# Kernel tuning notes

Measured on AMD Instinct MI355X. Metric: run time of the kernel, lower is better.

Reference implementation:

```python
import jax, jax.numpy as jnp
import numpy as np

B, T, V, D, C, O = 64, 128, 32, 128, 10000, 512


def setup_inputs() -> dict:
    key = jax.random.key(0)
    ks = jax.random.split(key, 14)
    s = 1.0 / np.sqrt(D)
    # ragged visit sequences: codes in [1, C), padded visits are all-zero codes
    codes = jax.random.randint(ks[0], (B, T, V), 1, C, dtype=jnp.int32)
    lengths = jax.random.randint(ks[1], (B,), 1, T + 1, dtype=jnp.int32)
    visit_mask = (jnp.arange(T)[None, :] < lengths[:, None])
    codes_x = codes * visit_mask[:, :, None].astype(jnp.int32)
    emb = (jax.random.normal(ks[2], (C, D), jnp.float32) * 0.02).at[0].set(0.0)
    return {
        "codes_x": codes_x,
        "emb": emb,
        "a_kernel": jax.random.normal(ks[3], (D, 3 * D), jnp.float32) * s,
        "a_rec": jax.random.normal(ks[4], (D, 3 * D), jnp.float32) * s,
        "a_bias": jnp.zeros((2, 3 * D), jnp.float32),
        "b_kernel": jax.random.normal(ks[5], (D, 3 * D), jnp.float32) * s,
        "b_rec": jax.random.normal(ks[6], (D, 3 * D), jnp.float32) * s,
        "b_bias": jnp.zeros((2, 3 * D), jnp.float32),
        "alpha_w": jax.random.normal(ks[7], (D, 1), jnp.float32) * s,
        "alpha_b": jnp.zeros((1,), jnp.float32),
        "beta_w": jax.random.normal(ks[8], (D, D), jnp.float32) * s,
        "beta_b": jnp.zeros((D,), jnp.float32),
        "cls_w": jax.random.normal(ks[9], (D, O), jnp.float32) * s,
        "cls_b": jnp.zeros((O,), jnp.float32),
    }


def gru(x, mask, kernel, rec, bias):
    """Keras GRU (reset_after=True), masked: carries state+output through padded steps.
    x: [B,T,D], mask: [B,T] bool -> [B,T,D]."""
    bi, br = bias[0], bias[1]
    xp = x @ kernel + bi  # [B,T,3D] precomputed input projection

    def step(h, inp):
        xp_t, m_t = inp
        hp = h @ rec + br
        xz, xr, xh = jnp.split(xp_t, 3, axis=-1)
        hz, hr, hh = jnp.split(hp, 3, axis=-1)
        z = jax.nn.sigmoid(xz + hz)
        r = jax.nn.sigmoid(xr + hr)
        hcand = jnp.tanh(xh + r * hh)
        h_new = z * h + (1.0 - z) * hcand
        h_out = jnp.where(m_t[:, None], h_new, h)
        return h_out, h_out

    h0 = jnp.zeros((x.shape[0], rec.shape[0]), x.dtype)
    _, ys = jax.lax.scan(step, h0, (jnp.swapaxes(xp, 0, 1), jnp.swapaxes(mask, 0, 1)))
    return jnp.swapaxes(ys, 0, 1)


def retain_forward(codes_x, emb, a_kernel, a_rec, a_bias, b_kernel, b_rec, b_bias,
                   alpha_w, alpha_b, beta_w, beta_b, cls_w, cls_b):
    x = emb[codes_x].sum(axis=2)                     # [B,T,D] visit embeddings
    mask = x.sum(axis=-1) != 0                       # [B,T] visit mask
    lengths = mask.sum(axis=-1)                      # [B]
    # masked reverse: rx[b, j] = x[b, lengths[b]-1-j] for j < lengths[b], else 0
    t = x.shape[1]
    idx = lengths[:, None] - 1 - jnp.arange(t)[None, :]  # [B,T]
    valid = idx >= 0
    rx = jnp.take_along_axis(x, jnp.clip(idx, 0, t - 1)[:, :, None], axis=1)
    rx = rx * valid[:, :, None].astype(x.dtype)
    # dual GRU attention (dropout inactive at inference)
    g = gru(rx, mask, a_kernel, a_rec, a_bias)
    h = gru(rx, mask, b_kernel, b_rec, b_bias)
    attn_alpha = jax.nn.softmax(g @ alpha_w + alpha_b, axis=1)   # [B,T,1]
    attn_beta = jnp.tanh(h @ beta_w + beta_b)                    # [B,T,D]
    c = jnp.sum(attn_alpha * attn_beta * x, axis=1)              # [B,D]
    return c @ cls_w + cls_b                                     # [B,O]


def reference(codes_x, emb, a_kernel, a_rec, a_bias, b_kernel, b_rec, b_bias,
              alpha_w, alpha_b, beta_w, beta_b, cls_w, cls_b):
    return retain_forward(codes_x, emb, a_kernel, a_rec, a_bias, b_kernel, b_rec,
                          b_bias, alpha_w, alpha_b, beta_w, beta_b, cls_w, cls_b)
```

## Files before the change

kernel.cpp:

```cpp
#include <hip/hip_runtime.h>
#include <math.h>

#define BATCH 64
#define TT 128
#define VV 32
#define DD 128
#define OO 512
#define N3 384
#define NN 768

#define OFF_X      0u
#define OFF_XPC    1048576u
#define OFF_GSEQ   7340032u
#define OFF_HSEQ   8388608u
#define OFF_INTS   9437184u
#define OFF_ALPHA  9453632u
#define OFF_CPART  9461824u

__global__ __launch_bounds__(128) void k_gather(const int* __restrict__ codes,
        const float* __restrict__ emb, float* __restrict__ x, int* __restrict__ mask) {
    int bt = blockIdx.x;
    int d = threadIdx.x;
    const int* cp = codes + (size_t)bt * VV;
    float acc = 0.f;
    #pragma unroll 8
    for (int v = 0; v < VV; ++v) {
        int code = cp[v];
        acc += emb[(size_t)code * DD + d];
    }
    x[(size_t)bt * DD + d] = acc;
    float s = acc;
    #pragma unroll
    for (int off = 32; off; off >>= 1) s += __shfl_xor(s, off);
    __shared__ float red[2];
    if ((d & 63) == 0) red[d >> 6] = s;
    __syncthreads();
    if (d == 0) mask[bt] = ((red[0] + red[1]) != 0.0f) ? 1 : 0;
}

__global__ __launch_bounds__(128) void k_len(const int* __restrict__ mask,
        int* __restrict__ lengths, int* __restrict__ ridx) {
    int b = blockIdx.x, t = threadIdx.x;
    int m = mask[b * TT + t];
    unsigned long long bal = __ballot(m != 0);
    __shared__ int cnt[2];
    if ((t & 63) == 0) cnt[t >> 6] = __popcll(bal);
    __syncthreads();
    int len = cnt[0] + cnt[1];
    if (t == 0) lengths[b] = len;
    ridx[b * TT + t] = len - 1 - t;
}

__global__ __launch_bounds__(256) void k_xp(const float* __restrict__ x,
        const float* __restrict__ akern, const float* __restrict__ bkern,
        const float* __restrict__ abias, const float* __restrict__ bbias,
        float* __restrict__ xpc) {
    __shared__ __attribute__((aligned(16))) float As[32][68];
    __shared__ __attribute__((aligned(16))) float Bs[32][68];
    int mb = blockIdx.x, nb = blockIdx.y;
    int n0 = nb * 64;
    int tid = threadIdx.x;
    int tx = tid & 15, ty = tid >> 4;
    float acc[4][4] = {};
    for (int k0 = 0; k0 < DD; k0 += 32) {
        #pragma unroll
        for (int i = 0; i < 2; ++i) {
            int s = tid * 2 + i;
            int row = s >> 3, kk = (s & 7) * 4;
            float4 v = *reinterpret_cast<const float4*>(x + (size_t)(mb * 64 + row) * DD + k0 + kk);
            As[kk][row] = v.x; As[kk+1][row] = v.y; As[kk+2][row] = v.z; As[kk+3][row] = v.w;
        }
        #pragma unroll
        for (int i = 0; i < 2; ++i) {
            int s = tid * 2 + i;
            int kk = s >> 4, c = (s & 15) * 4;
            int n = n0 + c;
            const float* src = (n < N3) ? (akern + (size_t)(k0 + kk) * N3 + n)
                                        : (bkern + (size_t)(k0 + kk) * N3 + (n - N3));
            *reinterpret_cast<float4*>(&Bs[kk][c]) = *reinterpret_cast<const float4*>(src);
        }
        __syncthreads();
        #pragma unroll
        for (int kk = 0; kk < 32; ++kk) {
            float4 a = *reinterpret_cast<const float4*>(&As[kk][ty * 4]);
            float4 bv = *reinterpret_cast<const float4*>(&Bs[kk][tx * 4]);
            float av[4] = {a.x, a.y, a.z, a.w};
            float bw[4] = {bv.x, bv.y, bv.z, bv.w};
            #pragma unroll
            for (int i2 = 0; i2 < 4; ++i2)
                #pragma unroll
                for (int j2 = 0; j2 < 4; ++j2)
                    acc[i2][j2] = fmaf(av[i2], bw[j2], acc[i2][j2]);
        }
        __syncthreads();
    }
    int nbase = n0 + tx * 4;
    float4 bias;
    if (nbase < N3) bias = *reinterpret_cast<const float4*>(abias + nbase);
    else            bias = *reinterpret_cast<const float4*>(bbias + (nbase - N3));
    #pragma unroll
    for (int i2 = 0; i2 < 4; ++i2) {
        int m = mb * 64 + ty * 4 + i2;
        float4 o;
        o.x = acc[i2][0] + bias.x; o.y = acc[i2][1] + bias.y;
        o.z = acc[i2][2] + bias.z; o.w = acc[i2][3] + bias.w;
        *reinterpret_cast<float4*>(xpc + (size_t)m * NN + nbase) = o;
    }
}

__device__ __forceinline__ float fast_sigmoid(float x) {
    return 1.f / (1.f + __expf(-x));
}
__device__ __forceinline__ float fast_tanh(float x) {
    float xc = fminf(fmaxf(x, -15.f), 15.f);
    float e2 = __expf(2.f * xc);
    return (e2 - 1.f) / (e2 + 1.f);
}

#define LOADW(i) float4 w##i; { const float* rp = rec + (size_t)(k0 + 4 * i) * N3 + j; \
    w##i.x = rp[0]; w##i.y = rp[N3]; w##i.z = rp[2 * N3]; w##i.w = rp[3 * N3]; }
#define DOTW(i) { float4 hv = *reinterpret_cast<const float4*>(&h_lds[k0 + 4 * i]); \
    a0 = fmaf(hv.x, w##i.x, a0); a1 = fmaf(hv.y, w##i.y, a1); \
    a2 = fmaf(hv.z, w##i.z, a2); a3 = fmaf(hv.w, w##i.w, a3); }

__global__ __launch_bounds__(768) __attribute__((amdgpu_waves_per_eu(3, 3)))
void k_gru(
        const float* __restrict__ arec, const float* __restrict__ abias,
        const float* __restrict__ brec, const float* __restrict__ bbias,
        const float* __restrict__ xpc, const int* __restrict__ mask,
        const int* __restrict__ ridx, float* __restrict__ gseq, float* __restrict__ hseq) {
    int b = blockIdx.x & 63;
    int gru = blockIdx.x >> 6;
    const float* rec  = gru ? brec : arec;
    const float* bias = gru ? bbias : abias;
    float* seq = gru ? hseq : gseq;
    int t = threadIdx.x;
    int half = (t >= N3) ? 1 : 0;
    int j = t - half * N3;
    int k0 = half * 64;
    LOADW(0)  LOADW(1)  LOADW(2)  LOADW(3)
    LOADW(4)  LOADW(5)  LOADW(6)  LOADW(7)
    LOADW(8)  LOADW(9)  LOADW(10) LOADW(11)
    LOADW(12) LOADW(13) LOADW(14) LOADW(15)
    __shared__ __attribute__((aligned(16))) float h_lds[DD];
    __shared__ float part[768];
    __shared__ int smask[TT];
    __shared__ int sridx[TT];
    if (t < TT) { smask[t] = mask[b * TT + t]; sridx[t] = ridx[b * TT + t]; }
    if (t < DD) h_lds[t] = 0.f;
    float bz_r = 0.f, br_r = 0.f, bh_r = 0.f, bz_i = 0.f, br_i = 0.f, bh_i = 0.f;
    if (t < DD) {
        bz_r = bias[N3 + t];  br_r = bias[N3 + DD + t];  bh_r = bias[N3 + 2 * DD + t];
        bz_i = bias[t];       br_i = bias[DD + t];       bh_i = bias[2 * DD + t];
    }
    float hreg = 0.f;
    __syncthreads();
    const float* xpb = xpc + (size_t)b * TT * NN + gru * N3;
    for (int step = 0; step < TT; ++step) {
        int m = smask[step];
        if (!m) {
            if (t < DD) seq[(size_t)(b * TT + step) * DD + t] = hreg;
            continue;
        }
        float xz = 0.f, xr = 0.f, xh = 0.f;
        if (t < DD) {
            int row = sridx[step];
            if (row >= 0) {
                const float* xrow = xpb + (size_t)row * NN;
                xz = xrow[t]; xr = xrow[DD + t]; xh = xrow[2 * DD + t];
            } else {
                xz = bz_i; xr = br_i; xh = bh_i;
            }
        }
        float a0 = 0.f, a1 = 0.f, a2 = 0.f, a3 = 0.f;
        DOTW(0)  DOTW(1)  DOTW(2)  DOTW(3)
        DOTW(4)  DOTW(5)  DOTW(6)  DOTW(7)
        DOTW(8)  DOTW(9)  DOTW(10) DOTW(11)
        DOTW(12) DOTW(13) DOTW(14) DOTW(15)
        part[t] = (a0 + a1) + (a2 + a3);
        __syncthreads();
        if (t < DD) {
            float hz = part[t]           + part[t + N3]          + bz_r;
            float hr = part[t + DD]      + part[t + N3 + DD]     + br_r;
            float hh = part[t + 2 * DD]  + part[t + N3 + 2 * DD] + bh_r;
            float z = fast_sigmoid(xz + hz);
            float r = fast_sigmoid(xr + hr);
            float hc = fast_tanh(xh + r * hh);
            float hnew = z * hreg + (1.f - z) * hc;
            hreg = hnew;
            h_lds[t] = hnew;
            seq[(size_t)(b * TT + step) * DD + t] = hnew;
        }
        __syncthreads();
    }
}

__global__ __launch_bounds__(128) void k_alpha(const float* __restrict__ gseq,
        const float* __restrict__ alpha_w, const float* __restrict__ alpha_b,
        float* __restrict__ alpha) {
    int b = blockIdx.x, t = threadIdx.x;
    __shared__ float aw[DD];
    aw[t] = alpha_w[t];
    __syncthreads();
    const float* g = gseq + (size_t)(b * TT + t) * DD;
    float acc = 0.f;
    #pragma unroll
    for (int k = 0; k < DD; k += 4) {
        float4 gv = *reinterpret_cast<const float4*>(g + k);
        acc = fmaf(gv.x, aw[k],     acc);
        acc = fmaf(gv.y, aw[k + 1], acc);
        acc = fmaf(gv.z, aw[k + 2], acc);
        acc = fmaf(gv.w, aw[k + 3], acc);
    }
    float logit = acc + alpha_b[0];
    float mx = logit;
    #pragma unroll
    for (int off = 32; off; off >>= 1) mx = fmaxf(mx, __shfl_xor(mx, off));
    __shared__ float redm[2];
    if ((t & 63) == 0) redm[t >> 6] = mx;
    __syncthreads();
    mx = fmaxf(redm[0], redm[1]);
    float e = expf(logit - mx);
    float s = e;
    #pragma unroll
    for (int off = 32; off; off >>= 1) s += __shfl_xor(s, off);
    __shared__ float reds[2];
    if ((t & 63) == 0) reds[t >> 6] = s;
    __syncthreads();
    alpha[b * TT + t] = e / (reds[0] + reds[1]);
}

__global__ __launch_bounds__(128) void k_beta(const float* __restrict__ hseq,
        const float* __restrict__ x, const float* __restrict__ beta_w,
        const float* __restrict__ beta_b, const float* __restrict__ alpha,
        float* __restrict__ cpart) {
    __shared__ __attribute__((aligned(16))) float bw[DD][DD];
    __shared__ __attribute__((aligned(16))) float hr[4][DD];
    __shared__ float cred[4][DD];
    int b = blockIdx.x >> 3, grp = blockIdx.x & 7;
    int tid = threadIdx.x;
    for (int i = tid; i < DD * DD / 4; i += 128) {
        float4 v = *reinterpret_cast<const float4*>(beta_w + (size_t)i * 4);
        *reinterpret_cast<float4*>(&bw[0][0] + (size_t)i * 4) = v;
    }
    int trow = tid >> 5, dq = (tid & 31) * 4;
    float bb0 = beta_b[dq], bb1 = beta_b[dq + 1], bb2 = beta_b[dq + 2], bb3 = beta_b[dq + 3];
    float c0 = 0.f, c1 = 0.f, c2 = 0.f, c3 = 0.f;
    for (int tg = 0; tg < 4; ++tg) {
        int t = grp * 16 + tg * 4 + trow;
        size_t rowoff = (size_t)(b * TT + t) * DD;
        float4 hv = *reinterpret_cast<const float4*>(hseq + rowoff + dq);
        __syncthreads();
        *reinterpret_cast<float4*>(&hr[trow][dq]) = hv;
        __syncthreads();
        float a0 = 0.f, a1 = 0.f, a2 = 0.f, a3 = 0.f;
        #pragma unroll 8
        for (int k = 0; k < DD; ++k) {
            float hk = hr[trow][k];
            float4 w = *reinterpret_cast<const float4*>(&bw[k][dq]);
            a0 = fmaf(hk, w.x, a0); a1 = fmaf(hk, w.y, a1);
            a2 = fmaf(hk, w.z, a2); a3 = fmaf(hk, w.w, a3);
        }
        float al = alpha[b * TT + t];
        float4 xv = *reinterpret_cast<const float4*>(x + rowoff + dq);
        c0 = fmaf(al * tanhf(a0 + bb0), xv.x, c0);
        c1 = fmaf(al * tanhf(a1 + bb1), xv.y, c1);
        c2 = fmaf(al * tanhf(a2 + bb2), xv.z, c2);
        c3 = fmaf(al * tanhf(a3 + bb3), xv.w, c3);
    }
    cred[trow][dq] = c0; cred[trow][dq + 1] = c1;
    cred[trow][dq + 2] = c2; cred[trow][dq + 3] = c3;
    __syncthreads();
    if (tid < 32) {
        #pragma unroll
        for (int i = 0; i < 4; ++i) {
            int d = tid * 4 + i;
            float sum = cred[0][d] + cred[1][d] + cred[2][d] + cred[3][d];
            cpart[(size_t)(b * 8 + grp) * DD + d] = sum;
        }
    }
}

__global__ __launch_bounds__(256) void k_out(const float* __restrict__ cpart,
        const float* __restrict__ cls_w, const float* __restrict__ cls_b,
        float* __restrict__ out) {
    __shared__ float cl[DD];
    int b = blockIdx.x, tid = threadIdx.x;
    if (tid < DD) {
        float s = 0.f;
        #pragma unroll
        for (int p = 0; p < 8; ++p) s += cpart[(size_t)(b * 8 + p) * DD + tid];
        cl[tid] = s;
    }
    __syncthreads();
    #pragma unroll
    for (int rep = 0; rep < 2; ++rep) {
        int o = tid + rep * 256;
        float acc = cls_b[o];
        #pragma unroll 8
        for (int k = 0; k < DD; ++k)
            acc = fmaf(cl[k], cls_w[(size_t)k * OO + o], acc);
        out[(size_t)b * OO + o] = acc;
    }
}

extern "C" void kernel_launch(void* const* d_in, const int* in_sizes, int n_in,
                              void* d_out, int out_size, void* d_ws, size_t ws_size,
                              hipStream_t stream) {
    const int*   codes   = (const int*)d_in[0];
    const float* emb     = (const float*)d_in[1];
    const float* akern   = (const float*)d_in[2];
    const float* arec    = (const float*)d_in[3];
    const float* abias   = (const float*)d_in[4];
    const float* bkern   = (const float*)d_in[5];
    const float* brec    = (const float*)d_in[6];
    const float* bbias   = (const float*)d_in[7];
    const float* alpha_w = (const float*)d_in[8];
    const float* alpha_b = (const float*)d_in[9];
    const float* beta_w  = (const float*)d_in[10];
    const float* beta_b  = (const float*)d_in[11];
    const float* cls_w   = (const float*)d_in[12];
    const float* cls_b   = (const float*)d_in[13];
    float* ws   = (float*)d_ws;
    float* x    = ws + OFF_X;
    float* xpc  = ws + OFF_XPC;
    float* gseq = ws + OFF_GSEQ;
    float* hseq = ws + OFF_HSEQ;
    int*   ints = (int*)(ws + OFF_INTS);
    int* mask    = ints;
    int* ridx    = ints + 8192;
    int* lengths = ints + 16384;
    float* alpha = ws + OFF_ALPHA;
    float* cpart = ws + OFF_CPART;
    float* out   = (float*)d_out;

    k_gather<<<BATCH * TT, 128, 0, stream>>>(codes, emb, x, mask);
    k_len<<<BATCH, 128, 0, stream>>>(mask, lengths, ridx);
    dim3 g3(128, 12);
    k_xp<<<g3, 256, 0, stream>>>(x, akern, bkern, abias, bbias, xpc);
    k_gru<<<128, 768, 0, stream>>>(arec, abias, brec, bbias, xpc, mask, ridx, gseq, hseq);
    k_alpha<<<BATCH, 128, 0, stream>>>(gseq, alpha_w, alpha_b, alpha);
    k_beta<<<BATCH * 8, 128, 0, stream>>>(hseq, x, beta_w, beta_b, alpha, cpart);
    k_out<<<BATCH, 256, 0, stream>>>(cpart, cls_w, cls_b, out);
}
```

Measured before the change: 188.5 us.

## Retile GRU recurrent matvec into 4-column by 16-row register blocks

Each thread now holds a 16x4 block of the recurrent weights, loaded as float4 rows, instead of a 64x1 column slice. Each h vector value read from LDS is reused across four output columns. The K dimension is split 8 ways instead of 2, so the partial-sum buffer grows to 8 slices and the gate threads reduce 8 partials per gate. This cuts LDS reads of h per step and makes the weight loads coalesced, at the cost of a longer reduction on the serial critical path.

```diff
diff --git a/kernel.cpp b/kernel.cpp
--- a/kernel.cpp
+++ b/kernel.cpp
@@ -117,13 +117,21 @@
     return (e2 - 1.f) / (e2 + 1.f);
 }
 
-#define LOADW(i) float4 w##i; { const float* rp = rec + (size_t)(k0 + 4 * i) * N3 + j; \
-    w##i.x = rp[0]; w##i.y = rp[N3]; w##i.z = rp[2 * N3]; w##i.w = rp[3 * N3]; }
-#define DOTW(i) { float4 hv = *reinterpret_cast<const float4*>(&h_lds[k0 + 4 * i]); \
-    a0 = fmaf(hv.x, w##i.x, a0); a1 = fmaf(hv.y, w##i.y, a1); \
-    a2 = fmaf(hv.z, w##i.z, a2); a3 = fmaf(hv.w, w##i.w, a3); }
-
-__global__ __launch_bounds__(768) __attribute__((amdgpu_waves_per_eu(3, 3)))
+#define LOADW(i) \
+    float4 w##i = *reinterpret_cast<const float4*>(rec + (size_t)(krow0 + i) * N3 + j4); \
+    asm volatile("" : "+v"(w##i.x), "+v"(w##i.y), "+v"(w##i.z), "+v"(w##i.w));
+#define DOTQ(q, i0, i1, i2, i3) { \
+    float4 hv = *reinterpret_cast<const float4*>(&h_lds[krow0 + 4 * (q)]); \
+    acc.x = fmaf(hv.x, w##i0.x, acc.x); acc.y = fmaf(hv.x, w##i0.y, acc.y); \
+    acc.z = fmaf(hv.x, w##i0.z, acc.z); acc.w = fmaf(hv.x, w##i0.w, acc.w); \
+    acc.x = fmaf(hv.y, w##i1.x, acc.x); acc.y = fmaf(hv.y, w##i1.y, acc.y); \
+    acc.z = fmaf(hv.y, w##i1.z, acc.z); acc.w = fmaf(hv.y, w##i1.w, acc.w); \
+    acc.x = fmaf(hv.z, w##i2.x, acc.x); acc.y = fmaf(hv.z, w##i2.y, acc.y); \
+    acc.z = fmaf(hv.z, w##i2.z, acc.z); acc.w = fmaf(hv.z, w##i2.w, acc.w); \
+    acc.x = fmaf(hv.w, w##i3.x, acc.x); acc.y = fmaf(hv.w, w##i3.y, acc.y); \
+    acc.z = fmaf(hv.w, w##i3.z, acc.z); acc.w = fmaf(hv.w, w##i3.w, acc.w); }
+
+__global__ __launch_bounds__(768, 3)
 void k_gru(
         const float* __restrict__ arec, const float* __restrict__ abias,
         const float* __restrict__ brec, const float* __restrict__ bbias,
@@ -135,15 +143,16 @@
     const float* bias = gru ? bbias : abias;
     float* seq = gru ? hseq : gseq;
     int t = threadIdx.x;
-    int half = (t >= N3) ? 1 : 0;
-    int j = t - half * N3;
-    int k0 = half * 64;
+    int c4 = t % 96;
+    int kc = t / 96;
+    int j4 = c4 * 4;
+    int krow0 = kc * 16;
     LOADW(0)  LOADW(1)  LOADW(2)  LOADW(3)
     LOADW(4)  LOADW(5)  LOADW(6)  LOADW(7)
     LOADW(8)  LOADW(9)  LOADW(10) LOADW(11)
     LOADW(12) LOADW(13) LOADW(14) LOADW(15)
     __shared__ __attribute__((aligned(16))) float h_lds[DD];
-    __shared__ float part[768];
+    __shared__ __attribute__((aligned(16))) float part[8 * N3];
     __shared__ int smask[TT];
     __shared__ int sridx[TT];
     if (t < TT) { smask[t] = mask[b * TT + t]; sridx[t] = ridx[b * TT + t]; }
@@ -172,17 +181,21 @@
                 xz = bz_i; xr = br_i; xh = bh_i;
             }
         }
-        float a0 = 0.f, a1 = 0.f, a2 = 0.f, a3 = 0.f;
-        DOTW(0)  DOTW(1)  DOTW(2)  DOTW(3)
-        DOTW(4)  DOTW(5)  DOTW(6)  DOTW(7)
-        DOTW(8)  DOTW(9)  DOTW(10) DOTW(11)
-        DOTW(12) DOTW(13) DOTW(14) DOTW(15)
-        part[t] = (a0 + a1) + (a2 + a3);
+        float4 acc = {0.f, 0.f, 0.f, 0.f};
+        DOTQ(0, 0, 1, 2, 3)
+        DOTQ(1, 4, 5, 6, 7)
+        DOTQ(2, 8, 9, 10, 11)
+        DOTQ(3, 12, 13, 14, 15)
+        *reinterpret_cast<float4*>(&part[kc * N3 + j4]) = acc;
         __syncthreads();
         if (t < DD) {
-            float hz = part[t]           + part[t + N3]          + bz_r;
-            float hr = part[t + DD]      + part[t + N3 + DD]     + br_r;
-            float hh = part[t + 2 * DD]  + part[t + N3 + 2 * DD] + bh_r;
+            float hz = bz_r, hr = br_r, hh = bh_r;
+            #pragma unroll
+            for (int g = 0; g < 8; ++g) {
+                hz += part[g * N3 + t];
+                hr += part[g * N3 + DD + t];
+                hh += part[g * N3 + 2 * DD + t];
+            }
             float z = fast_sigmoid(xz + hz);
             float r = fast_sigmoid(xr + hr);
             float hc = fast_tanh(xh + r * hh);
```

Result: faster. 170.7 us (-9.5%).
